# Optimization experiments

Measured on AMD Instinct MI355X. Metric: run time of the kernel, lower is better.

The kernel has to match this reference:

```python
import jax, jax.numpy as jnp
import numpy as np

B, S, D, H, F = 2, 2048, 1024, 16, 64  # batch, seq, d_model, heads, head_dim


def setup_inputs() -> dict:
    key = jax.random.key(0)
    ks = jax.random.split(key, 7)
    return {
        "q": jax.random.normal(ks[0], (B, S, D), dtype=jnp.float32),
        "k": jax.random.normal(ks[1], (B, S, D), dtype=jnp.float32),
        "v": jax.random.normal(ks[2], (B, S, D), dtype=jnp.float32),
        "Wq": jax.random.normal(ks[3], (H, D, F), dtype=jnp.float32) * 0.02,
        "Wk": jax.random.normal(ks[4], (H, D, F), dtype=jnp.float32) * 0.02,
        "Wv": jax.random.normal(ks[5], (H, D, F), dtype=jnp.float32) * 0.02,
        "Wo": jax.random.normal(ks[6], (H * F, D), dtype=jnp.float32) * 0.02,
    }


def reference(q, k, v, Wq, Wk, Wv, Wo):
    head_dim = Wq.shape[-1]
    queries = jnp.einsum('bqo,hof->bhqf', q, Wq)
    keys = jnp.einsum('bko,hof->bhkf', k, Wk)
    values = jnp.einsum('bvo,hof->bhvf', v, Wv)
    # K.batch_dot(queries, keys, axes=[3,3]) -> [b,h,q,k]
    scores = jnp.einsum('bhqf,bhkf->bhqk', queries, keys) / jnp.sqrt(
        jnp.asarray(head_dim, dtype=queries.dtype))
    attn = jax.nn.softmax(scores, axis=-1)
    # Faithful to K.batch_dot(attn, values, axes=[2,2]):
    # contracts the QUERY axis of attn with the seq axis of values -> A^T V
    out4 = jnp.einsum('bhqk,bhqf->bhkf', attn, values)  # [b,h,s,f]
    b = out4.shape[0]
    # Faithful raw reshape [b,h,s,f] -> [b,s,h*f] (no transpose, as in original)
    out = out4.reshape(b, out4.shape[2], -1)
    return out @ Wo  # [b,s,d_model]
```

## Files before the change

kernel.cpp:

```cpp
#include <hip/hip_runtime.h>
#include <hip/hip_bf16.h>
#include <stdint.h>

#define Bc 2
#define Sc 2048
#define Dc 1024
#define Hc 16
#define Fc 64
constexpr int BHSF = Bc * Hc * Sc * Fc;

typedef __attribute__((ext_vector_type(8))) short bf16x8;
typedef __attribute__((ext_vector_type(4))) float f32x4;

#define MFMA16(a, b, c) __builtin_amdgcn_mfma_f32_16x16x32_bf16(a, b, c, 0, 0, 0)
#define EXP2(x) __builtin_amdgcn_exp2f(x)
#define SCALE2 0.18033688f

__device__ inline short f2bfn(float x) {
    __hip_bfloat16 h = __float2bfloat16(x);
    return __builtin_bit_cast(short, h);
}
__device__ inline uint32_t cvt2(float lo, float hi) {
    uint32_t a = (uint16_t)f2bfn(lo);
    uint32_t b = (uint16_t)f2bfn(hi);
    return a | (b << 16);
}
__device__ inline float bf2f(short s) {
    uint32_t u = ((uint32_t)(uint16_t)s) << 16;
    return __builtin_bit_cast(float, u);
}

__device__ inline void dma16(const short* g, short* l) {
    __builtin_amdgcn_global_load_lds(
        (const __attribute__((address_space(1))) void*)g,
        (__attribute__((address_space(3))) void*)(uintptr_t)(uint32_t)(uintptr_t)l,
        16, 0, 0);
}

__global__ __launch_bounds__(256) void xcvt_kernel(
    const float* __restrict__ a, const float* __restrict__ b,
    const float* __restrict__ c, short* __restrict__ out)
{
    const float* src = (blockIdx.y == 0) ? a : (blockIdx.y == 1) ? b : c;
    const size_t base = (size_t)blockIdx.x * 4096 + threadIdx.x * 16;
    const float* s = src + base;
    short* d = out + (size_t)blockIdx.y * 4096 * 1024 + base;
    f32x4 v0 = ((const f32x4*)s)[0], v1 = ((const f32x4*)s)[1];
    f32x4 v2 = ((const f32x4*)s)[2], v3 = ((const f32x4*)s)[3];
    bf16x8 p0, p1;
    #pragma unroll
    for (int i = 0; i < 4; ++i) {
        p0[i] = f2bfn(v0[i]); p0[4 + i] = f2bfn(v1[i]);
        p1[i] = f2bfn(v2[i]); p1[4 + i] = f2bfn(v3[i]);
    }
    *(bf16x8*)d       = p0;
    *(bf16x8*)(d + 8) = p1;
}

__global__ __launch_bounds__(256) void tcvt_all_kernel(
    const float* __restrict__ Wq, const float* __restrict__ Wk,
    const float* __restrict__ Wv, const float* __restrict__ Wo,
    short* __restrict__ WqT, short* __restrict__ WkT,
    short* __restrict__ WvT, short* __restrict__ WoT)
{
    __shared__ short td[64 * 72];
    const int t = threadIdx.x;
    const int sr = t >> 2, sc = (t & 3) * 16;
    const int zp = blockIdx.z;
    const int m0 = blockIdx.x * 64;

    const float* in; short* out; int N, n0;
    if (zp < 48) {
        const int sel = zp >> 4, h = zp & 15;
        in  = ((sel == 0) ? Wq : (sel == 1) ? Wk : Wv) + (size_t)h * Dc * Fc;
        out = ((sel == 0) ? WqT : (sel == 1) ? WkT : WvT) + (size_t)h * Fc * Dc;
        N = Fc; n0 = 0;
    } else {
        in = Wo; out = WoT; N = Dc; n0 = (zp - 48) * 64;
    }

    const float* src = in + (size_t)(m0 + sr) * N + n0 + sc;
    #pragma unroll
    for (int i = 0; i < 16; i += 4) {
        f32x4 a = *(const f32x4*)(src + i);
        td[sr * 72 + sc + i + 0] = f2bfn(a[0]);
        td[sr * 72 + sc + i + 1] = f2bfn(a[1]);
        td[sr * 72 + sc + i + 2] = f2bfn(a[2]);
        td[sr * 72 + sc + i + 3] = f2bfn(a[3]);
    }
    __syncthreads();
    alignas(16) short vals[16];
    #pragma unroll
    for (int i = 0; i < 16; ++i) vals[i] = td[(sc + i) * 72 + sr];
    short* dst = out + (size_t)(n0 + sr) * Dc + m0 + sc;
    *(bf16x8*)dst       = *(const bf16x8*)&vals[0];
    *(bf16x8*)(dst + 8) = *(const bf16x8*)&vals[8];
}

__global__ __launch_bounds__(256) void proj_kernel(
    const short* __restrict__ Xb,
    const short* __restrict__ WqT, const short* __restrict__ WkT,
    const short* __restrict__ WvT,
    short* __restrict__ Qo, short* __restrict__ Ko, short* __restrict__ VtO)
{
    const int mt = blockIdx.x, hp = blockIdx.y, z = blockIdx.z;
    const short* X  = Xb + (size_t)z * 4096 * Dc;
    const short* Wt = ((z == 0) ? WqT : (z == 1) ? WkT : WvT) + (size_t)hp * 128 * Dc;
    const int m0 = mt * 128;

    __shared__ short sm[2][8192];

    const int t = threadIdx.x, lane = t & 63, w = t >> 6;
    const int wm = w >> 1, wn = w & 1;
    const int l15 = lane & 15, g = lane >> 4;
    const int lr = lane >> 2, lc = (lane & 3) * 8;

    auto issue = [&](int buf, int d0) {
        #pragma unroll
        for (int i = 0; i < 2; ++i) {
            const int rr = (w * 2 + i) * 16 + lr;
            dma16(&X [(size_t)(m0 + rr) * Dc + d0 + lc],
                  &sm[buf][(w * 2 + i) * 512]);
            dma16(&Wt[(size_t)rr        * Dc + d0 + lc],
                  &sm[buf][4096 + (w * 2 + i) * 512]);
        }
    };

    f32x4 acc[4][4];
    #pragma unroll
    for (int i = 0; i < 4; ++i)
        #pragma unroll
        for (int j = 0; j < 4; ++j) acc[i][j] = (f32x4){0.f, 0.f, 0.f, 0.f};

    issue(0, 0);

    for (int d0 = 0; d0 < Dc; d0 += 32) {
        const int cur = (d0 >> 5) & 1;
        __syncthreads();
        if (d0 + 32 < Dc) issue(cur ^ 1, d0 + 32);
        const short* xb = &sm[cur][0];
        const short* wb = &sm[cur][4096];
        bf16x8 afr[4], bfr[4];
        #pragma unroll
        for (int ms = 0; ms < 4; ++ms)
            afr[ms] = *(const bf16x8*)&xb[(wm * 64 + ms * 16 + l15) * 32 + g * 8];
        #pragma unroll
        for (int fb = 0; fb < 4; ++fb)
            bfr[fb] = *(const bf16x8*)&wb[(wn * 64 + fb * 16 + l15) * 32 + g * 8];
        #pragma unroll
        for (int ms = 0; ms < 4; ++ms)
            #pragma unroll
            for (int fb = 0; fb < 4; ++fb)
                acc[ms][fb] = MFMA16(afr[ms], bfr[fb], acc[ms][fb]);
    }

    short* ob = &sm[0][0];
    const float oscale = (z == 0) ? SCALE2 : 1.0f;
    const int b = m0 >> 11, s0 = m0 & 2047;
    #pragma unroll
    for (int p = 0; p < 2; ++p) {
        __syncthreads();
        if (wn == p) {
            #pragma unroll
            for (int ms = 0; ms < 4; ++ms)
                #pragma unroll
                for (int fb = 0; fb < 4; ++fb)
                    #pragma unroll
                    for (int r = 0; r < 4; ++r)
                        ob[(wm * 64 + ms * 16 + g * 4 + r) * 72 + fb * 16 + l15] =
                            f2bfn(acc[ms][fb][r] * oscale);
        }
        __syncthreads();
        const int h = hp * 2 + p;
        if (z < 2) {
            const int row = t >> 1, c0 = (t & 1) * 32;
            short* outp = ((z == 0) ? Qo : Ko)
                        + ((size_t)(b * Hc + h) * Sc + s0 + row) * Fc + c0;
            #pragma unroll
            for (int j = 0; j < 32; j += 8)
                *(bf16x8*)&outp[j] = *(const bf16x8*)&ob[row * 72 + c0 + j];
        } else {
            const int f = t >> 2, cg = (t & 3) * 32;
            short* o = VtO + ((size_t)(b * Hc + h) * Fc + f) * Sc + s0 + cg;
            alignas(16) short vals[32];
            #pragma unroll
            for (int j = 0; j < 32; ++j) vals[j] = ob[(cg + j) * 72 + f];
            #pragma unroll
            for (int j = 0; j < 32; j += 8)
                *(bf16x8*)(o + j) = *(const bf16x8*)&vals[j];
        }
    }
}

__global__ __launch_bounds__(256) void stats_kernel(
    const short* __restrict__ Qg, const short* __restrict__ Kg,
    float* __restrict__ mrow)
{
    const int bh = blockIdx.x;
    const int q0 = blockIdx.y * 128;
    const short* Qb = Qg + (size_t)bh * Sc * Fc;
    const short* Kb = Kg + (size_t)bh * Sc * Fc;

    __shared__ short ksA[64 * 72], ksB[64 * 72];

    const int t = threadIdx.x, lane = t & 63, w = t >> 6;
    const int l15 = lane & 15, g = lane >> 4;
    const int sr4 = t >> 2, sc4 = (t & 3) * 16;

    bf16x8 qf[2][2];
    #pragma unroll
    for (int qs2 = 0; qs2 < 2; ++qs2)
        #pragma unroll
        for (int kc2 = 0; kc2 < 2; ++kc2)
            qf[qs2][kc2] = *(const bf16x8*)
                &Qb[(size_t)(q0 + w * 32 + qs2 * 16 + l15) * Fc + kc2 * 32 + g * 8];

    bf16x8 kr0, kr1;
    auto gload = [&](int kt) {
        const short* s = &Kb[(size_t)(kt + sr4) * Fc + sc4];
        kr0 = *(const bf16x8*)s;
        kr1 = *(const bf16x8*)(s + 8);
    };
    auto swrite = [&](short* d) {
        *(bf16x8*)&d[sr4 * 72 + sc4]     = kr0;
        *(bf16x8*)&d[sr4 * 72 + sc4 + 8] = kr1;
    };

    f32x4 ls[2];
    ls[0] = (f32x4){0.f, 0.f, 0.f, 0.f};
    ls[1] = (f32x4){0.f, 0.f, 0.f, 0.f};

    gload(0); swrite(ksA); gload(64);

    auto half = [&](int kt, const short* cur, short* nxt) {
        __syncthreads();
        if (kt + 64 < Sc) swrite(nxt);
        if (kt + 128 < Sc) gload(kt + 128);
        #pragma unroll
        for (int kf = 0; kf < 4; ++kf) {
            bf16x8 a0 = *(const bf16x8*)&cur[(kf * 16 + l15) * 72 + 0  + g * 8];
            bf16x8 a1 = *(const bf16x8*)&cur[(kf * 16 + l15) * 72 + 32 + g * 8];
            #pragma unroll
            for (int qs2 = 0; qs2 < 2; ++qs2) {
                f32x4 acc = (f32x4){0.f, 0.f, 0.f, 0.f};
                acc = MFMA16(a0, qf[qs2][0], acc);
                acc = MFMA16(a1, qf[qs2][1], acc);
                #pragma unroll
                for (int r = 0; r < 4; ++r) ls[qs2][r] += EXP2(acc[r]);
            }
        }
    };

    for (int kt = 0; kt < Sc; kt += 128) {
        half(kt,      ksA, ksB);
        half(kt + 64, ksB, ksA);
    }

    #pragma unroll
    for (int qs2 = 0; qs2 < 2; ++qs2) {
        float l = (ls[qs2][0] + ls[qs2][1]) + (ls[qs2][2] + ls[qs2][3]);
        l += __shfl_xor(l, 16, 64);
        l += __shfl_xor(l, 32, 64);
        if (lane < 16)
            mrow[bh * Sc + q0 + w * 32 + qs2 * 16 + l15] = __log2f(l);
    }
}

__global__ __launch_bounds__(256) void attn_kernel(
    const short* __restrict__ Qg, const short* __restrict__ Kg,
    const short* __restrict__ VtG, const float* __restrict__ mrow,
    short* __restrict__ O4a, short* __restrict__ O4b)
{
    const int bh = blockIdx.x;
    const int qh = blockIdx.y;
    const int k0 = blockIdx.z * 256;
    const int qbeg = qh * 1024, qend = qbeg + 1024;
    const short* Qb = Qg  + (size_t)bh * Sc * Fc;
    const short* Kb = Kg  + (size_t)bh * Sc * Fc;
    const short* Vb = VtG + (size_t)bh * Fc * Sc;
    const float* mb = mrow + (size_t)bh * Sc;

    __shared__ short qs[64 * 72];
    __shared__ short vt[64 * 72];
    __shared__ short pl[256 * 72];

    const int t = threadIdx.x, lane = t & 63, w = t >> 6;
    const int l15 = lane & 15, g = lane >> 4;
    const int sr8 = t >> 2, sc8 = (t & 3) * 16;

    bf16x8 kf[4][2];
    #pragma unroll
    for (int ks = 0; ks < 4; ++ks)
        #pragma unroll
        for (int kc = 0; kc < 2; ++kc)
            kf[ks][kc] = *(const bf16x8*)
                &Kb[(size_t)(k0 + w * 64 + ks * 16 + l15) * Fc + kc * 32 + g * 8];

    f32x4 oacc[4][4];
    #pragma unroll
    for (int i = 0; i < 4; ++i)
        #pragma unroll
        for (int j = 0; j < 4; ++j) oacc[i][j] = (f32x4){0.f, 0.f, 0.f, 0.f};

    bf16x8 qr0, qr1, vr0, vr1;
    auto gload = [&](int qn) {
        const short* s = &Qb[(size_t)(qn + sr8) * Fc + sc8];
        qr0 = *(const bf16x8*)s;
        qr1 = *(const bf16x8*)(s + 8);
        const short* v = &Vb[(size_t)sr8 * Sc + qn + sc8];
        vr0 = *(const bf16x8*)v;
        vr1 = *(const bf16x8*)(v + 8);
    };

    gload(qbeg);

    for (int q0 = qbeg; q0 < qend; q0 += 64) {
        __syncthreads();
        *(bf16x8*)&qs[sr8 * 72 + sc8]     = qr0;
        *(bf16x8*)&qs[sr8 * 72 + sc8 + 8] = qr1;
        *(bf16x8*)&vt[sr8 * 72 + sc8]     = vr0;
        *(bf16x8*)&vt[sr8 * 72 + sc8 + 8] = vr1;
        if (q0 + 64 < qend) gload(q0 + 64);
        f32x4 mq[4];
        #pragma unroll
        for (int qf = 0; qf < 4; ++qf)
            mq[qf] = *(const f32x4*)&mb[q0 + qf * 16 + g * 4];
        __syncthreads();

        #pragma unroll
        for (int qf = 0; qf < 4; ++qf) {
            bf16x8 qa0 = *(const bf16x8*)&qs[(qf * 16 + l15) * 72 + 0  + g * 8];
            bf16x8 qa1 = *(const bf16x8*)&qs[(qf * 16 + l15) * 72 + 32 + g * 8];
            #pragma unroll
            for (int ks = 0; ks < 4; ++ks) {
                f32x4 acc = (f32x4){0.f, 0.f, 0.f, 0.f};
                acc = MFMA16(qa0, kf[ks][0], acc);
                acc = MFMA16(qa1, kf[ks][1], acc);
                uint2 pv;
                pv.x = cvt2(EXP2(acc[0] - mq[qf][0]), EXP2(acc[1] - mq[qf][1]));
                pv.y = cvt2(EXP2(acc[2] - mq[qf][2]), EXP2(acc[3] - mq[qf][3]));
                *(uint2*)&pl[(w * 64 + ks * 16 + l15) * 72 + qf * 16 + g * 4] = pv;
            }
        }

        #pragma unroll
        for (int qc = 0; qc < 64; qc += 32) {
            bf16x8 pa[4], vbf[4];
            #pragma unroll
            for (int ks = 0; ks < 4; ++ks)
                pa[ks] = *(const bf16x8*)&pl[(w * 64 + ks * 16 + l15) * 72 + qc + g * 8];
            #pragma unroll
            for (int fb = 0; fb < 4; ++fb)
                vbf[fb] = *(const bf16x8*)&vt[(fb * 16 + l15) * 72 + qc + g * 8];
            #pragma unroll
            for (int ks = 0; ks < 4; ++ks)
                #pragma unroll
                for (int fb = 0; fb < 4; ++fb)
                    oacc[ks][fb] = MFMA16(pa[ks], vbf[fb], oacc[ks][fb]);
        }
    }

    __syncthreads();
    #pragma unroll
    for (int ks = 0; ks < 4; ++ks)
        #pragma unroll
        for (int fb = 0; fb < 4; ++fb)
            #pragma unroll
            for (int r = 0; r < 4; ++r)
                pl[(w * 64 + ks * 16 + g * 4 + r) * 72 + fb * 16 + l15] =
                    f2bfn(oacc[ks][fb][r]);
    __syncthreads();
    {
        short* O = qh ? O4b : O4a;
        short* o = O + ((size_t)bh * Sc + k0 + t) * Fc;
        #pragma unroll
        for (int j = 0; j < 64; j += 8)
            *(bf16x8*)&o[j] = *(const bf16x8*)&pl[t * 72 + j];
    }
}

__global__ __launch_bounds__(256) void outgemm_kernel(
    const short* __restrict__ Aa, const short* __restrict__ Ab,
    const short* __restrict__ WoT, float* __restrict__ out)
{
    const int m0 = blockIdx.x * 128, n0 = blockIdx.y * 64;

    __shared__ short asA[128 * 72], asB[128 * 72];
    __shared__ short wsA[64 * 72],  wsB[64 * 72];

    const int t = threadIdx.x, lane = t & 63, w = t >> 6;
    const int l15 = lane & 15, g = lane >> 4;
    const int ar = t >> 1, ac = (t & 1) * 32;
    const int wr = t >> 2, wc = (t & 3) * 16;

    bf16x8 ag0[4], ag1[4], wg[2];
    auto gload = [&](int d0) {
        const short* s0 = &Aa[(size_t)(m0 + ar) * Dc + d0 + ac];
        const short* s1 = &Ab[(size_t)(m0 + ar) * Dc + d0 + ac];
        #pragma unroll
        for (int j = 0; j < 4; ++j) { ag0[j] = *(const bf16x8*)(s0 + 8 * j);
                                      ag1[j] = *(const bf16x8*)(s1 + 8 * j); }
        const short* ww = &WoT[(size_t)(n0 + wr) * Dc + d0 + wc];
        wg[0] = *(const bf16x8*)ww;
        wg[1] = *(const bf16x8*)(ww + 8);
    };
    auto swrite = [&](short* asD, short* wsD) {
        #pragma unroll
        for (int j = 0; j < 4; ++j) {
            bf16x8 r;
            #pragma unroll
            for (int i = 0; i < 8; ++i)
                r[i] = f2bfn(bf2f(ag0[j][i]) + bf2f(ag1[j][i]));
            *(bf16x8*)&asD[ar * 72 + ac + 8 * j] = r;
        }
        *(bf16x8*)&wsD[wr * 72 + wc]     = wg[0];
        *(bf16x8*)&wsD[wr * 72 + wc + 8] = wg[1];
    };

    f32x4 acc[2][4];
    #pragma unroll
    for (int i = 0; i < 2; ++i)
        #pragma unroll
        for (int j = 0; j < 4; ++j) acc[i][j] = (f32x4){0.f, 0.f, 0.f, 0.f};

    gload(0); swrite(asA, wsA); gload(64);

    auto half = [&](int d0, const short* asC, const short* wsC,
                    short* asN, short* wsN) {
        __syncthreads();
        if (d0 + 64 < Dc) swrite(asN, wsN);
        if (d0 + 128 < Dc) gload(d0 + 128);
        #pragma unroll
        for (int kc = 0; kc < 64; kc += 32) {
            bf16x8 afr[2], bfr[4];
            #pragma unroll
            for (int ms = 0; ms < 2; ++ms)
                afr[ms] = *(const bf16x8*)&asC[(w * 32 + ms * 16 + l15) * 72 + kc + g * 8];
            #pragma unroll
            for (int nb = 0; nb < 4; ++nb)
                bfr[nb] = *(const bf16x8*)&wsC[(nb * 16 + l15) * 72 + kc + g * 8];
            #pragma unroll
            for (int ms = 0; ms < 2; ++ms)
                #pragma unroll
                for (int nb = 0; nb < 4; ++nb)
                    acc[ms][nb] = MFMA16(afr[ms], bfr[nb], acc[ms][nb]);
        }
    };

    for (int d0 = 0; d0 < Dc; d0 += 128) {
        half(d0,      asA, wsA, asB, wsB);
        half(d0 + 64, asB, wsB, asA, wsA);
    }

    #pragma unroll
    for (int ms = 0; ms < 2; ++ms)
        #pragma unroll
        for (int nb = 0; nb < 4; ++nb)
            #pragma unroll
            for (int r = 0; r < 4; ++r)
                out[(size_t)(m0 + w * 32 + ms * 16 + g * 4 + r) * 1024
                    + n0 + nb * 16 + l15] = acc[ms][nb][r];
}

extern "C" void kernel_launch(void* const* d_in, const int* in_sizes, int n_in,
                              void* d_out, int out_size, void* d_ws, size_t ws_size,
                              hipStream_t stream) {
    (void)in_sizes; (void)n_in; (void)out_size; (void)ws_size;
    const float* q  = (const float*)d_in[0];
    const float* k  = (const float*)d_in[1];
    const float* v  = (const float*)d_in[2];
    const float* Wq = (const float*)d_in[3];
    const float* Wk = (const float*)d_in[4];
    const float* Wv = (const float*)d_in[5];
    const float* Wo = (const float*)d_in[6];
    float* out = (float*)d_out;

    short* Xb  = (short*)d_ws;
    short* O4a = Xb;
    short* O4b = Xb + BHSF;
    short* Qw  = Xb  + (size_t)3 * 4096 * Dc;
    short* Kw  = Qw  + BHSF;
    short* Vt  = Kw  + BHSF;
    short* WqT = Vt  + BHSF;
    short* WkT = WqT + Hc * Dc * Fc;
    short* WvT = WkT + Hc * Dc * Fc;
    short* WoT = WvT + Hc * Dc * Fc;
    float* mw  = (float*)(WoT + Dc * Dc);

    xcvt_kernel<<<dim3(1024, 3), 256, 0, stream>>>(q, k, v, Xb);
    tcvt_all_kernel<<<dim3(16, 1, 64), 256, 0, stream>>>(Wq, Wk, Wv, Wo,
                                                         WqT, WkT, WvT, WoT);
    proj_kernel<<<dim3(32, 8, 3), 256, 0, stream>>>(Xb, WqT, WkT, WvT,
                                                    Qw, Kw, Vt);
    stats_kernel<<<dim3(32, 16), 256, 0, stream>>>(Qw, Kw, mw);
    attn_kernel<<<dim3(32, 2, 8), 256, 0, stream>>>(Qw, Kw, Vt, mw, O4a, O4b);
    outgemm_kernel<<<dim3(32, 16), 256, 0, stream>>>(O4a, O4b, WoT, out);
}
```

Measured before the change: 166.0 us.

## Load Q and V fragments directly into registers, removing shared staging and barriers

The attention kernel stops staging Q and V tiles through shared memory. Each wave now loads its MFMA operand fragments straight from global memory into registers, double-buffered one tile ahead, which removes both __syncthreads per 64-query step and leaves each wave's P buffer as private LDS. Launch bounds ask for 2 blocks per SM. In exchange every wave redundantly fetches the same Q/V data from global/L2 with narrower, strided accesses, and register pressure rises from the doubled fragment buffers.

```diff
diff --git a/kernel.cpp b/kernel.cpp
--- a/kernel.cpp
+++ b/kernel.cpp
@@ -266,7 +266,7 @@
     }
 }
 
-__global__ __launch_bounds__(256) void attn_kernel(
+__global__ __launch_bounds__(256, 2) void attn_kernel(
     const short* __restrict__ Qg, const short* __restrict__ Kg,
     const short* __restrict__ VtG, const float* __restrict__ mrow,
     short* __restrict__ O4a, short* __restrict__ O4b)
@@ -280,13 +280,11 @@
     const short* Vb = VtG + (size_t)bh * Fc * Sc;
     const float* mb = mrow + (size_t)bh * Sc;
 
-    __shared__ short qs[64 * 72];
-    __shared__ short vt[64 * 72];
-    __shared__ short pl[256 * 72];
+    __shared__ short pl[4][64 * 72];
 
     const int t = threadIdx.x, lane = t & 63, w = t >> 6;
     const int l15 = lane & 15, g = lane >> 4;
-    const int sr8 = t >> 2, sc8 = (t & 3) * 16;
+    short* plw = &pl[w][0];
 
     bf16x8 kf[4][2];
     #pragma unroll
@@ -296,67 +294,82 @@
             kf[ks][kc] = *(const bf16x8*)
                 &Kb[(size_t)(k0 + w * 64 + ks * 16 + l15) * Fc + kc * 32 + g * 8];
 
+    const short* qbase = Qb + (size_t)l15 * Fc + g * 8;
+    const short* vbase = Vb + (size_t)l15 * Sc + g * 8;
+
     f32x4 oacc[4][4];
     #pragma unroll
     for (int i = 0; i < 4; ++i)
         #pragma unroll
         for (int j = 0; j < 4; ++j) oacc[i][j] = (f32x4){0.f, 0.f, 0.f, 0.f};
 
-    bf16x8 qr0, qr1, vr0, vr1;
-    auto gload = [&](int qn) {
-        const short* s = &Qb[(size_t)(qn + sr8) * Fc + sc8];
-        qr0 = *(const bf16x8*)s;
-        qr1 = *(const bf16x8*)(s + 8);
-        const short* v = &Vb[(size_t)sr8 * Sc + qn + sc8];
-        vr0 = *(const bf16x8*)v;
-        vr1 = *(const bf16x8*)(v + 8);
-    };
-
-    gload(qbeg);
+    bf16x8 qa[4][2], qaN[4][2];
+    bf16x8 vf[2][4], vfN[2][4];
+    f32x4  mq[4],    mqN[4];
+
+    auto loadQ = [&](int q0, bf16x8 (&dq)[4][2], f32x4 (&dm)[4]) {
+        #pragma unroll
+        for (int qf = 0; qf < 4; ++qf) {
+            const short* s = qbase + (size_t)(q0 + qf * 16) * Fc;
+            dq[qf][0] = *(const bf16x8*)s;
+            dq[qf][1] = *(const bf16x8*)(s + 32);
+            dm[qf] = *(const f32x4*)&mb[q0 + qf * 16 + g * 4];
+        }
+    };
+    auto loadV = [&](int q0, bf16x8 (&dv)[2][4]) {
+        #pragma unroll
+        for (int c = 0; c < 2; ++c)
+            #pragma unroll
+            for (int fb = 0; fb < 4; ++fb)
+                dv[c][fb] = *(const bf16x8*)
+                    (vbase + (size_t)fb * 16 * Sc + q0 + c * 32);
+    };
+
+    loadQ(qbeg, qa, mq);
+    loadV(qbeg, vf);
 
     for (int q0 = qbeg; q0 < qend; q0 += 64) {
-        __syncthreads();
-        *(bf16x8*)&qs[sr8 * 72 + sc8]     = qr0;
-        *(bf16x8*)&qs[sr8 * 72 + sc8 + 8] = qr1;
-        *(bf16x8*)&vt[sr8 * 72 + sc8]     = vr0;
-        *(bf16x8*)&vt[sr8 * 72 + sc8 + 8] = vr1;
-        if (q0 + 64 < qend) gload(q0 + 64);
-        f32x4 mq[4];
-        #pragma unroll
-        for (int qf = 0; qf < 4; ++qf)
-            mq[qf] = *(const f32x4*)&mb[q0 + qf * 16 + g * 4];
-        __syncthreads();
+        if (q0 + 64 < qend) { loadQ(q0 + 64, qaN, mqN); loadV(q0 + 64, vfN); }
 
         #pragma unroll
         for (int qf = 0; qf < 4; ++qf) {
-            bf16x8 qa0 = *(const bf16x8*)&qs[(qf * 16 + l15) * 72 + 0  + g * 8];
-            bf16x8 qa1 = *(const bf16x8*)&qs[(qf * 16 + l15) * 72 + 32 + g * 8];
             #pragma unroll
             for (int ks = 0; ks < 4; ++ks) {
                 f32x4 acc = (f32x4){0.f, 0.f, 0.f, 0.f};
-                acc = MFMA16(qa0, kf[ks][0], acc);
-                acc = MFMA16(qa1, kf[ks][1], acc);
+                acc = MFMA16(qa[qf][0], kf[ks][0], acc);
+                acc = MFMA16(qa[qf][1], kf[ks][1], acc);
                 uint2 pv;
                 pv.x = cvt2(EXP2(acc[0] - mq[qf][0]), EXP2(acc[1] - mq[qf][1]));
                 pv.y = cvt2(EXP2(acc[2] - mq[qf][2]), EXP2(acc[3] - mq[qf][3]));
-                *(uint2*)&pl[(w * 64 + ks * 16 + l15) * 72 + qf * 16 + g * 4] = pv;
+                *(uint2*)&plw[(ks * 16 + l15) * 72 + qf * 16 + g * 4] = pv;
             }
         }
 
         #pragma unroll
-        for (int qc = 0; qc < 64; qc += 32) {
-            bf16x8 pa[4], vbf[4];
+        for (int qc = 0; qc < 2; ++qc) {
+            bf16x8 pa[4];
             #pragma unroll
             for (int ks = 0; ks < 4; ++ks)
-                pa[ks] = *(const bf16x8*)&pl[(w * 64 + ks * 16 + l15) * 72 + qc + g * 8];
-            #pragma unroll
-            for (int fb = 0; fb < 4; ++fb)
-                vbf[fb] = *(const bf16x8*)&vt[(fb * 16 + l15) * 72 + qc + g * 8];
+                pa[ks] = *(const bf16x8*)&plw[(ks * 16 + l15) * 72 + qc * 32 + g * 8];
             #pragma unroll
             for (int ks = 0; ks < 4; ++ks)
                 #pragma unroll
                 for (int fb = 0; fb < 4; ++fb)
-                    oacc[ks][fb] = MFMA16(pa[ks], vbf[fb], oacc[ks][fb]);
+                    oacc[ks][fb] = MFMA16(pa[ks], vf[qc][fb], oacc[ks][fb]);
+        }
+
+        if (q0 + 64 < qend) {
+            #pragma unroll
+            for (int qf = 0; qf < 4; ++qf) {
+                qa[qf][0] = qaN[qf][0];
+                qa[qf][1] = qaN[qf][1];
+                mq[qf]    = mqN[qf];
+            }
+            #pragma unroll
+            for (int c = 0; c < 2; ++c)
+                #pragma unroll
+                for (int fb = 0; fb < 4; ++fb)
+                    vf[c][fb] = vfN[c][fb];
         }
     }
 
@@ -367,15 +380,16 @@
         for (int fb = 0; fb < 4; ++fb)
             #pragma unroll
             for (int r = 0; r < 4; ++r)
-                pl[(w * 64 + ks * 16 + g * 4 + r) * 72 + fb * 16 + l15] =
+                plw[(ks * 16 + g * 4 + r) * 72 + fb * 16 + l15] =
                     f2bfn(oacc[ks][fb][r]);
     __syncthreads();
     {
+        const short* plf = &pl[0][0];
         short* O = qh ? O4b : O4a;
         short* o = O + ((size_t)bh * Sc + k0 + t) * Fc;
         #pragma unroll
         for (int j = 0; j < 64; j += 8)
-            *(bf16x8*)&o[j] = *(const bf16x8*)&pl[t * 72 + j];
+            *(bf16x8*)&o[j] = *(const bf16x8*)&plf[t * 72 + j];
     }
 }
 
```

New measurement: 224.6 us. 35.3% more time.
